# Performance work log

Hardware: AMD Instinct MI355X
Metric: run time of the kernel (lower is better)

## Reference

```python
import jax, jax.numpy as jnp
import numpy as np

B, N, DIM, HEADS, DIM_HEAD = 2, 2048, 1024, 16, 64
INNER = HEADS * DIM_HEAD  # 1024
SCALE = DIM_HEAD ** -0.5
EPS = 1e-5  # fp32 path in the source


def _layernorm_seq(x, g):
    # Faithful to the repo's LayerNorm: statistics over dim=1 (sequence axis),
    # unbiased=False variance, clamp(min=eps).rsqrt(), scale by g over last axis.
    mean = jnp.mean(x, axis=1, keepdims=True)            # [b,1,d]
    var = jnp.mean((x - mean) ** 2, axis=1, keepdims=True)
    return (x - mean) * jax.lax.rsqrt(jnp.maximum(var, EPS)) * g


def setup_inputs() -> dict:
    key = jax.random.key(0)
    ks = jax.random.split(key, 5)
    x = jax.random.normal(ks[0], (B, N, DIM), dtype=jnp.float32)
    rel_pos_bias = jax.random.normal(ks[1], (1, HEADS, N, N), dtype=jnp.float32)
    g = jnp.ones((DIM,), dtype=jnp.float32)
    wq = jax.random.normal(ks[2], (INNER, DIM), dtype=jnp.float32) * (DIM ** -0.5)
    wkv = jax.random.normal(ks[3], (2 * INNER, DIM), dtype=jnp.float32) * (DIM ** -0.5)
    wout = jax.random.normal(ks[4], (DIM, INNER), dtype=jnp.float32) * (INNER ** -0.5)
    return {"x": x, "rel_pos_bias": rel_pos_bias, "g": g, "wq": wq, "wkv": wkv, "wout": wout}


def reference(x, rel_pos_bias, g, wq, wkv, wout):
    # self-attention path: context = x, framerate = None
    xn = _layernorm_seq(x, g)           # [b,n,d]
    cn = xn                              # context is None -> same tensor, same norm
    q = jnp.einsum('bnd,ed->bne', xn, wq)        # [b,n,inner]
    kv = jnp.einsum('bnd,ed->bne', cn, wkv)      # [b,n,2*inner]
    k, v = jnp.split(kv, 2, axis=-1)
    def heads(t):
        return t.reshape(B, N, HEADS, DIM_HEAD).transpose(0, 2, 1, 3)  # b h n d
    q, k, v = heads(q) * SCALE, heads(k), heads(v)
    sim = jnp.einsum('bhid,bhjd->bhij', q, k) + rel_pos_bias
    attn = jax.nn.softmax(sim, axis=-1)
    out = jnp.einsum('bhij,bhjd->bhid', attn, v)
    out = out.transpose(0, 2, 1, 3).reshape(B, N, INNER)  # b n (h d)
    return jnp.einsum('bne,de->bnd', out, wout)
```

## Files before the change

kernel.cpp:

```cpp
#include <hip/hip_runtime.h>
#include <hip/hip_bf16.h>
#include <stdint.h>

#define B_ 2
#define N_ 2048
#define DIM_ 1024
#define HEADS_ 16
#define DH_ 64
#define EPS_ 1e-5f

typedef __attribute__((ext_vector_type(4))) float f32x4;
typedef __attribute__((ext_vector_type(8))) float f32x8;
typedef __attribute__((ext_vector_type(16))) float f32x16;
typedef __attribute__((ext_vector_type(8))) __bf16 bf16x8;
typedef __attribute__((ext_vector_type(4))) unsigned int u32x4;
typedef __attribute__((ext_vector_type(2))) unsigned int u32x2;

__device__ __forceinline__ f32x4 mfma16(bf16x8 a, bf16x8 b, f32x4 c) {
  return __builtin_amdgcn_mfma_f32_16x16x32_bf16(a, b, c, 0, 0, 0);
}

__device__ __forceinline__ f32x16 mfma32(bf16x8 a, bf16x8 b, f32x16 c) {
  return __builtin_amdgcn_mfma_f32_32x32x16_bf16(a, b, c, 0, 0, 0);
}

__device__ __forceinline__ unsigned short f2bf(float x) {
  unsigned int u = __builtin_bit_cast(unsigned int, x);
  u += 0x7fffu + ((u >> 16) & 1u);
  return (unsigned short)(u >> 16);
}

__device__ __forceinline__ unsigned int cvt_pk_bf16(float lo, float hi) {
  unsigned int r;
  asm("v_cvt_pk_bf16_f32 %0, %1, %2" : "=v"(r) : "v"(lo), "v"(hi));
  return r;
}

__device__ __forceinline__ float uasf(unsigned int u) { return __builtin_bit_cast(float, u); }
__device__ __forceinline__ unsigned int fasu(float f) { return __builtin_bit_cast(unsigned int, f); }

__device__ __forceinline__ bf16x8 ld_frag(const unsigned short* p) {
  u32x4 v = *reinterpret_cast<const u32x4*>(p);
  return __builtin_bit_cast(bf16x8, v);
}

__device__ __forceinline__ void gload_lds16(const unsigned short* g, unsigned short* l) {
  __builtin_amdgcn_global_load_lds((const __attribute__((address_space(1))) void*)g,
                                   (__attribute__((address_space(3))) void*)l, 16, 0, 0);
}

__global__ __launch_bounds__(256) void ln_part(const float* __restrict__ x,
                                               float* __restrict__ ps,
                                               float* __restrict__ pss) {
  const int d = blockIdx.x * 256 + threadIdx.x;
  const int b = blockIdx.y >> 4, sp = blockIdx.y & 15;
  const float* xp = x + (size_t)(b * N_ + sp * 128) * DIM_ + d;
  float s = 0.f, ss = 0.f;
  for (int i = 0; i < 128; ++i) {
    float v = xp[(size_t)i * DIM_];
    s += v;
    ss += v * v;
  }
  int c = b * DIM_ + d;
  ps[sp * (B_ * DIM_) + c] = s;
  pss[sp * (B_ * DIM_) + c] = ss;
}

__global__ void ln_fin(const float* __restrict__ ps, const float* __restrict__ pss,
                       const float* __restrict__ g, float* __restrict__ meanA,
                       float* __restrict__ sclA) {
  int c = blockIdx.x * 256 + threadIdx.x;
  float s = 0.f, ss = 0.f;
#pragma unroll
  for (int sp = 0; sp < 16; ++sp) {
    s += ps[sp * (B_ * DIM_) + c];
    ss += pss[sp * (B_ * DIM_) + c];
  }
  float m = s * (1.f / N_);
  float v = ss * (1.f / N_) - m * m;
  meanA[c] = m;
  sclA[c] = rsqrtf(fmaxf(v, EPS_)) * g[c & (DIM_ - 1)];
}

__global__ __launch_bounds__(256) void ln_apply(const float* __restrict__ x,
                                                const float* __restrict__ meanA,
                                                const float* __restrict__ sclA,
                                                unsigned short* __restrict__ xn) {
  size_t t = (size_t)blockIdx.x * 256 + threadIdx.x;
  size_t base = t * 8;
  int d0 = (int)(base & (DIM_ - 1));
  int b = base >= (size_t)N_ * DIM_;
  int c = b * DIM_ + d0;
  const float4* xp = reinterpret_cast<const float4*>(x + base);
  const float4* mp = reinterpret_cast<const float4*>(meanA + c);
  const float4* sp = reinterpret_cast<const float4*>(sclA + c);
  float4 x0 = xp[0], x1 = xp[1];
  float4 m0 = mp[0], m1 = mp[1];
  float4 s0 = sp[0], s1 = sp[1];
  union {
    unsigned short u[8];
    u32x4 v;
  } o;
  o.u[0] = f2bf((x0.x - m0.x) * s0.x);
  o.u[1] = f2bf((x0.y - m0.y) * s0.y);
  o.u[2] = f2bf((x0.z - m0.z) * s0.z);
  o.u[3] = f2bf((x0.w - m0.w) * s0.w);
  o.u[4] = f2bf((x1.x - m1.x) * s1.x);
  o.u[5] = f2bf((x1.y - m1.y) * s1.y);
  o.u[6] = f2bf((x1.z - m1.z) * s1.z);
  o.u[7] = f2bf((x1.w - m1.w) * s1.w);
  *reinterpret_cast<u32x4*>(xn + base) = o.v;
}

__global__ __launch_bounds__(256) void cast_bf16(const float* __restrict__ src,
                                                 unsigned short* __restrict__ dst, float scale) {
  size_t t = (size_t)blockIdx.x * 256 + threadIdx.x;
  size_t base = t * 8;
  const float4* sp = reinterpret_cast<const float4*>(src + base);
  float4 a = sp[0], b4 = sp[1];
  union {
    unsigned short u[8];
    u32x4 v;
  } o;
  o.u[0] = f2bf(a.x * scale);
  o.u[1] = f2bf(a.y * scale);
  o.u[2] = f2bf(a.z * scale);
  o.u[3] = f2bf(a.w * scale);
  o.u[4] = f2bf(b4.x * scale);
  o.u[5] = f2bf(b4.y * scale);
  o.u[6] = f2bf(b4.z * scale);
  o.u[7] = f2bf(b4.w * scale);
  *reinterpret_cast<u32x4*>(dst + base) = o.v;
}

template <bool OUT_F32>
__global__ __launch_bounds__(256) void gemm_bt(const unsigned short* __restrict__ A,
                                               const unsigned short* __restrict__ W,
                                               void* __restrict__ Cout, int K, int ldc) {
  __shared__ unsigned short sA[128 * 64];
  __shared__ unsigned short sB[128 * 64];
  const int tid = threadIdx.x, lane = tid & 63, w = tid >> 6;
  const int wm = w >> 1, wn = w & 1;
  const int l15 = lane & 15, l4 = lane >> 4;
  const int m0 = blockIdx.y * 128, n0 = blockIdx.x * 128;
  f32x4 acc[4][4] = {};
  for (int kt = 0; kt < K; kt += 64) {
    __syncthreads();
#pragma unroll
    for (int p = 0; p < 4; ++p) {
      int flat = p * 256 + tid;
      int row = flat >> 3, c = flat & 7;
      int cs = c ^ (row & 7);
      gload_lds16(A + (size_t)(m0 + row) * K + kt + cs * 8, sA + (size_t)(p * 256 + w * 64) * 8);
      gload_lds16(W + (size_t)(n0 + row) * K + kt + cs * 8, sB + (size_t)(p * 256 + w * 64) * 8);
    }
    __syncthreads();
#pragma unroll
    for (int kk = 0; kk < 2; ++kk) {
      bf16x8 af[4], bfr[4];
#pragma unroll
      for (int i = 0; i < 4; ++i) {
        int rowA = wm * 64 + i * 16 + l15;
        af[i] = ld_frag(sA + rowA * 64 + (((kk * 4 + l4) ^ (rowA & 7)) * 8));
        int rowB = wn * 64 + i * 16 + l15;
        bfr[i] = ld_frag(sB + rowB * 64 + (((kk * 4 + l4) ^ (rowB & 7)) * 8));
      }
#pragma unroll
      for (int i = 0; i < 4; ++i)
#pragma unroll
        for (int j = 0; j < 4; ++j) acc[i][j] = mfma16(af[i], bfr[j], acc[i][j]);
    }
  }
#pragma unroll
  for (int i = 0; i < 4; ++i)
#pragma unroll
    for (int j = 0; j < 4; ++j)
#pragma unroll
      for (int r = 0; r < 4; ++r) {
        size_t off =
            (size_t)(m0 + wm * 64 + i * 16 + l4 * 4 + r) * ldc + (n0 + wn * 64 + j * 16 + l15);
        if (OUT_F32)
          ((float*)Cout)[off] = acc[i][j][r];
        else
          ((unsigned short*)Cout)[off] = f2bf(acc[i][j][r]);
      }
}

__global__ __launch_bounds__(256) void transpose_v(const unsigned short* __restrict__ qkv,
                                                   unsigned short* __restrict__ Vt) {
  __shared__ unsigned short tt[64][65];
  const int tid = threadIdx.x;
  const int h = blockIdx.y >> 1, b = blockIdx.y & 1;
  const int n0 = blockIdx.x * 64;
  const unsigned short* src = qkv + (size_t)(b * N_ + n0) * 3072 + 2048 + h * 64;
#pragma unroll
  for (int i = 0; i < 16; ++i) {
    int idx = i * 256 + tid;
    int r = idx >> 6, c = idx & 63;
    tt[r][c] = src[(size_t)r * 3072 + c];
  }
  __syncthreads();
  unsigned short* dst = Vt + (size_t)(b * HEADS_ + h) * 64 * N_ + n0;
#pragma unroll
  for (int i = 0; i < 16; ++i) {
    int idx = i * 256 + tid;
    int dh = idx >> 6, nn = idx & 63;
    dst[(size_t)dh * N_ + nn] = tt[nn][dh];
  }
}

__global__ __launch_bounds__(512, 2) void flash_attn(const unsigned short* __restrict__ qkv,
                                                     const float* __restrict__ bias,
                                                     const unsigned short* __restrict__ Vt,
                                                     unsigned short* __restrict__ Oatt) {
  __shared__ unsigned short sK[128 * 64];
  __shared__ unsigned short sV[64 * 128];
  __shared__ float sBias[8][32 * 128];

  const int tid = threadIdx.x, lane = tid & 63, w = tid >> 6;
  const int l31 = lane & 31, hi = lane >> 5;
  const int r = blockIdx.x;
  const int bh = r & 31, iblk = r >> 5;
  const int h = bh & 15, b = bh >> 4;
  const int qbase = iblk * 256 + w * 32;

  const unsigned short* Kg = qkv + (size_t)b * N_ * 3072 + 1024 + h * 64;
  const unsigned short* VtB = Vt + (size_t)(b * HEADS_ + h) * 64 * N_;
  const float* bias_h = bias + (size_t)h * N_ * N_;

  const int kflat0 = tid, kflat1 = 512 + tid;
  const int krow0 = kflat0 >> 3, kc0 = (kflat0 & 7) ^ (krow0 & 7);
  const int krow1 = kflat1 >> 3, kc1 = (kflat1 & 7) ^ (krow1 & 7);
  const int vrow0 = kflat0 >> 4, vc0 = (kflat0 & 15) ^ (vrow0 & 15);
  const int vrow1 = kflat1 >> 4, vc1 = (kflat1 & 15) ^ (vrow1 & 15);
  unsigned short* sKb0 = sK + (size_t)(w * 64) * 8;
  unsigned short* sKb1 = sK + (size_t)(512 + w * 64) * 8;
  unsigned short* sVb0 = sV + (size_t)(w * 64) * 8;
  unsigned short* sVb1 = sV + (size_t)(512 + w * 64) * 8;

#define STAGE_KV(JN)                                                       \
  gload_lds16(Kg + (size_t)((JN) + krow0) * 3072 + kc0 * 8, sKb0);         \
  gload_lds16(Kg + (size_t)((JN) + krow1) * 3072 + kc1 * 8, sKb1);         \
  gload_lds16(VtB + (size_t)vrow0 * N_ + (JN) + vc0 * 8, sVb0);            \
  gload_lds16(VtB + (size_t)vrow1 * N_ + (JN) + vc1 * 8, sVb1);

  float* sBw = sBias[w];
  unsigned short* sBw_us = reinterpret_cast<unsigned short*>(sBw);
  const int brr = lane >> 5, bsl = lane & 31;
  const float* bQ = bias_h + (size_t)qbase * N_;
#define SBI(i, JN)                                                            \
  gload_lds16((const unsigned short*)(bQ + (size_t)(2 * (i) + brr) * N_ +     \
                                      (JN) + ((bsl ^ (2 * (i) + brr)) << 2)), \
              sBw_us + (i) * 512);
#define STAGE_BIAS(JN)                                                     \
  SBI(0, JN) SBI(1, JN) SBI(2, JN) SBI(3, JN) SBI(4, JN) SBI(5, JN)        \
  SBI(6, JN) SBI(7, JN) SBI(8, JN) SBI(9, JN) SBI(10, JN) SBI(11, JN)      \
  SBI(12, JN) SBI(13, JN) SBI(14, JN) SBI(15, JN)

#define LDBIAS(DST, CB)                                                        \
  {                                                                            \
    const float* myB_ = sBw + l31 * 128;                                       \
    f32x4 t0 = *reinterpret_cast<const f32x4*>(myB_ + ((((CB) + 0 + hi) ^ l31) << 2)); \
    f32x4 t1 = *reinterpret_cast<const f32x4*>(myB_ + ((((CB) + 2 + hi) ^ l31) << 2)); \
    f32x4 t2 = *reinterpret_cast<const f32x4*>(myB_ + ((((CB) + 4 + hi) ^ l31) << 2)); \
    f32x4 t3 = *reinterpret_cast<const f32x4*>(myB_ + ((((CB) + 6 + hi) ^ l31) << 2)); \
    f32x8 u0_ = __builtin_shufflevector(t0, t1, 0, 1, 2, 3, 4, 5, 6, 7);       \
    f32x8 u1_ = __builtin_shufflevector(t2, t3, 0, 1, 2, 3, 4, 5, 6, 7);       \
    DST = __builtin_shufflevector(u0_, u1_, 0, 1, 2, 3, 4, 5, 6, 7, 8, 9, 10,  \
                                  11, 12, 13, 14, 15);                         \
  }

#define FRAGK(OUT, ROWB, CH)                                              \
  {                                                                       \
    int row_ = (ROWB) + l31;                                              \
    OUT = ld_frag(sK + row_ * 64 + (((CH) ^ (row_ & 7)) * 8));            \
  }
#define FRAGV(OUT, ROWB, CH)                                              \
  {                                                                       \
    int row_ = (ROWB) + l31;                                              \
    OUT = ld_frag(sV + row_ * 128 + (((CH) ^ (row_ & 15)) * 8));          \
  }

#define PACK2(S, PLO, PHI)                                                 \
  {                                                                        \
    unsigned int w0 = cvt_pk_bf16(S[0], S[1]), w1 = cvt_pk_bf16(S[2], S[3]);     \
    unsigned int w2 = cvt_pk_bf16(S[4], S[5]), w3 = cvt_pk_bf16(S[6], S[7]);     \
    unsigned int w4 = cvt_pk_bf16(S[8], S[9]), w5 = cvt_pk_bf16(S[10], S[11]);   \
    unsigned int w6 = cvt_pk_bf16(S[12], S[13]), w7 = cvt_pk_bf16(S[14], S[15]); \
    auto rA = __builtin_amdgcn_permlane32_swap(w0, w2, false, false);      \
    auto rB = __builtin_amdgcn_permlane32_swap(w1, w3, false, false);      \
    auto rC = __builtin_amdgcn_permlane32_swap(w4, w6, false, false);      \
    auto rD = __builtin_amdgcn_permlane32_swap(w5, w7, false, false);      \
    u32x4 pw;                                                              \
    pw[0] = rA[0]; pw[1] = rB[0]; pw[2] = rA[1]; pw[3] = rB[1];            \
    PLO = __builtin_bit_cast(bf16x8, pw);                                  \
    pw[0] = rC[0]; pw[1] = rD[0]; pw[2] = rC[1]; pw[3] = rD[1];            \
    PHI = __builtin_bit_cast(bf16x8, pw);                                  \
  }

  bf16x8 qf0, qf1, qf2, qf3;
  {
    const unsigned short* Qg =
        qkv + (size_t)(b * N_ + qbase + l31) * 3072 + h * 64 + hi * 8;
    qf0 = ld_frag(Qg);
    qf1 = ld_frag(Qg + 16);
    qf2 = ld_frag(Qg + 32);
    qf3 = ld_frag(Qg + 48);
  }

  f32x16 o0 = {}, o1 = {};
  float m_run = -1e30f, l_run = 0.f;

  STAGE_KV(0)
  STAGE_BIAS(0)

  const int NP = N_ / 128;
  for (int p = 0; p < NP; ++p) {
    asm volatile("s_waitcnt vmcnt(0) lgkmcnt(0)" ::: "memory");
    __builtin_amdgcn_s_barrier();

    f32x16 SA0, SA1, SB0, SB1;
    LDBIAS(SA0, 0)
    LDBIAS(SA1, 8)
    LDBIAS(SB0, 16)
    LDBIAS(SB1, 24)
    asm volatile("s_waitcnt lgkmcnt(0)" ::: "memory");
    __builtin_amdgcn_sched_barrier(0);

    if (p + 1 < NP) {
      const size_t jn = (size_t)(p + 1) * 128;
      STAGE_BIAS(jn)
    }

    __builtin_amdgcn_s_setprio(1);
    {
      bf16x8 kf;
      FRAGK(kf, 0, 0 + hi)  SA0 = mfma32(kf, qf0, SA0);
      FRAGK(kf, 0, 2 + hi)  SA0 = mfma32(kf, qf1, SA0);
      FRAGK(kf, 0, 4 + hi)  SA0 = mfma32(kf, qf2, SA0);
      FRAGK(kf, 0, 6 + hi)  SA0 = mfma32(kf, qf3, SA0);
      FRAGK(kf, 32, 0 + hi) SA1 = mfma32(kf, qf0, SA1);
      FRAGK(kf, 32, 2 + hi) SA1 = mfma32(kf, qf1, SA1);
      FRAGK(kf, 32, 4 + hi) SA1 = mfma32(kf, qf2, SA1);
      FRAGK(kf, 32, 6 + hi) SA1 = mfma32(kf, qf3, SA1);
      FRAGK(kf, 64, 0 + hi) SB0 = mfma32(kf, qf0, SB0);
      FRAGK(kf, 64, 2 + hi) SB0 = mfma32(kf, qf1, SB0);
      FRAGK(kf, 64, 4 + hi) SB0 = mfma32(kf, qf2, SB0);
      FRAGK(kf, 64, 6 + hi) SB0 = mfma32(kf, qf3, SB0);
      FRAGK(kf, 96, 0 + hi) SB1 = mfma32(kf, qf0, SB1);
      FRAGK(kf, 96, 2 + hi) SB1 = mfma32(kf, qf1, SB1);
      FRAGK(kf, 96, 4 + hi) SB1 = mfma32(kf, qf2, SB1);
      FRAGK(kf, 96, 6 + hi) SB1 = mfma32(kf, qf3, SB1);
    }
    __builtin_amdgcn_s_setprio(0);

    float c0 = SA0[0], c1 = SA1[0], c2 = SB0[0], c3 = SB1[0];
#pragma unroll
    for (int i = 1; i < 16; ++i) {
      c0 = fmaxf(c0, SA0[i]);
      c1 = fmaxf(c1, SA1[i]);
      c2 = fmaxf(c2, SB0[i]);
      c3 = fmaxf(c3, SB1[i]);
    }
    float mx = fmaxf(fmaxf(c0, c1), fmaxf(c2, c3));
    {
      auto pr_ = __builtin_amdgcn_permlane32_swap(fasu(mx), fasu(mx), false, false);
      mx = fmaxf(uasf(pr_[0]), uasf(pr_[1]));
    }
    float mn = fmaxf(m_run, mx);
    float alpha = __expf(m_run - mn);
#pragma unroll
    for (int i = 0; i < 16; ++i) {
      SA0[i] = __expf(SA0[i] - mn);
      SA1[i] = __expf(SA1[i] - mn);
      SB0[i] = __expf(SB0[i] - mn);
      SB1[i] = __expf(SB1[i] - mn);
    }
    float r0 = 0.f, r1 = 0.f, r2 = 0.f, r3 = 0.f;
#pragma unroll
    for (int i = 0; i < 16; ++i) {
      r0 += SA0[i];
      r1 += SA1[i];
      r2 += SB0[i];
      r3 += SB1[i];
    }
    float rs = (r0 + r1) + (r2 + r3);
    {
      auto pr_ = __builtin_amdgcn_permlane32_swap(fasu(rs), fasu(rs), false, false);
      rs = uasf(pr_[0]) + uasf(pr_[1]);
    }
    l_run = l_run * alpha + rs;
    m_run = mn;
#pragma unroll
    for (int i = 0; i < 16; ++i) {
      o0[i] *= alpha;
      o1[i] *= alpha;
    }

    bf16x8 pA0, pA1, pA2, pA3, pB0, pB1, pB2, pB3;
    PACK2(SA0, pA0, pA1)
    PACK2(SA1, pA2, pA3)
    PACK2(SB0, pB0, pB1)
    PACK2(SB1, pB2, pB3)

    __builtin_amdgcn_s_setprio(1);
    {
      bf16x8 vf;
      FRAGV(vf, 0, 0 + hi)   o0 = mfma32(vf, pA0, o0);
      FRAGV(vf, 0, 2 + hi)   o0 = mfma32(vf, pA1, o0);
      FRAGV(vf, 0, 4 + hi)   o0 = mfma32(vf, pA2, o0);
      FRAGV(vf, 0, 6 + hi)   o0 = mfma32(vf, pA3, o0);
      FRAGV(vf, 0, 8 + hi)   o0 = mfma32(vf, pB0, o0);
      FRAGV(vf, 0, 10 + hi)  o0 = mfma32(vf, pB1, o0);
      FRAGV(vf, 0, 12 + hi)  o0 = mfma32(vf, pB2, o0);
      FRAGV(vf, 0, 14 + hi)  o0 = mfma32(vf, pB3, o0);
      FRAGV(vf, 32, 0 + hi)  o1 = mfma32(vf, pA0, o1);
      FRAGV(vf, 32, 2 + hi)  o1 = mfma32(vf, pA1, o1);
      FRAGV(vf, 32, 4 + hi)  o1 = mfma32(vf, pA2, o1);
      FRAGV(vf, 32, 6 + hi)  o1 = mfma32(vf, pA3, o1);
      FRAGV(vf, 32, 8 + hi)  o1 = mfma32(vf, pB0, o1);
      FRAGV(vf, 32, 10 + hi) o1 = mfma32(vf, pB1, o1);
      FRAGV(vf, 32, 12 + hi) o1 = mfma32(vf, pB2, o1);
      FRAGV(vf, 32, 14 + hi) o1 = mfma32(vf, pB3, o1);
    }
    __builtin_amdgcn_s_setprio(0);

    asm volatile("s_waitcnt lgkmcnt(0)" ::: "memory");
    __builtin_amdgcn_s_barrier();
    if (p + 1 < NP) {
      const size_t jn = (size_t)(p + 1) * 128;
      STAGE_KV(jn)
    }
  }
#undef STAGE_KV
#undef SBI
#undef STAGE_BIAS
#undef LDBIAS
#undef FRAGK
#undef FRAGV
#undef PACK2

  float inv = 1.f / l_run;
  unsigned short* orow =
      Oatt + (size_t)(b * N_ + qbase + l31) * 1024 + h * 64 + hi * 4;
#pragma unroll
  for (int g = 0; g < 4; ++g) {
    u32x2 pk0;
    pk0[0] = cvt_pk_bf16(o0[g * 4 + 0] * inv, o0[g * 4 + 1] * inv);
    pk0[1] = cvt_pk_bf16(o0[g * 4 + 2] * inv, o0[g * 4 + 3] * inv);
    *reinterpret_cast<u32x2*>(orow + g * 8) = pk0;
    u32x2 pk1;
    pk1[0] = cvt_pk_bf16(o1[g * 4 + 0] * inv, o1[g * 4 + 1] * inv);
    pk1[1] = cvt_pk_bf16(o1[g * 4 + 2] * inv, o1[g * 4 + 3] * inv);
    *reinterpret_cast<u32x2*>(orow + 32 + g * 8) = pk1;
  }
}

extern "C" void kernel_launch(void* const* d_in, const int* in_sizes, int n_in, void* d_out,
                              int out_size, void* d_ws, size_t ws_size, hipStream_t stream) {
  const float* x = (const float*)d_in[0];
  const float* bias = (const float*)d_in[1];
  const float* g = (const float*)d_in[2];
  const float* wq = (const float*)d_in[3];
  const float* wkv = (const float*)d_in[4];
  const float* wout = (const float*)d_in[5];
  float* out = (float*)d_out;

  float* ps = (float*)d_ws;
  float* pss = ps + 16 * B_ * DIM_;
  float* meanA = pss + 16 * B_ * DIM_;
  float* sclA = meanA + B_ * DIM_;
  unsigned short* xn = (unsigned short*)(sclA + B_ * DIM_);
  unsigned short* Wqkv = xn + (size_t)4096 * 1024;
  unsigned short* WoutB = Wqkv + (size_t)3072 * 1024;
  unsigned short* qkvb = WoutB + (size_t)1024 * 1024;
  unsigned short* Vt = qkvb + (size_t)4096 * 3072;
  unsigned short* Oatt = xn;

  ln_part<<<dim3(DIM_ / 256, B_ * 16), 256, 0, stream>>>(x, ps, pss);
  ln_fin<<<dim3((B_ * DIM_) / 256), 256, 0, stream>>>(ps, pss, g, meanA, sclA);
  ln_apply<<<dim3((B_ * N_ * DIM_) / 2048), 256, 0, stream>>>(x, meanA, sclA, xn);
  cast_bf16<<<dim3((DIM_ * DIM_) / 2048), 256, 0, stream>>>(wq, Wqkv, 0.125f);
  cast_bf16<<<dim3((2 * DIM_ * DIM_) / 2048), 256, 0, stream>>>(wkv, Wqkv + (size_t)DIM_ * DIM_,
                                                                1.0f);
  cast_bf16<<<dim3((DIM_ * DIM_) / 2048), 256, 0, stream>>>(wout, WoutB, 1.0f);
  gemm_bt<false><<<dim3(3072 / 128, 4096 / 128), 256, 0, stream>>>(xn, Wqkv, qkvb, DIM_, 3072);
  transpose_v<<<dim3(N_ / 64, B_ * HEADS_), 256, 0, stream>>>(qkvb, Vt);
  flash_attn<<<dim3(256), 512, 0, stream>>>(qkvb, bias, Vt, Oatt);
  gemm_bt<true><<<dim3(1024 / 128, 4096 / 128), 256, 0, stream>>>(Oatt, WoutB, out, DIM_, 1024);
}
```

Measured before the change: 173.8 us.

## Double-buffer LDS tiles in gemm_bt to overlap global loads with MFMA

Changes the GEMM main loop to keep two LDS stages. The next K-tile is prefetched with direct-to-LDS loads while MFMAs consume the current one, and each iteration ends with a single waitcnt plus barrier. This targets the exposed global-load latency in the projection GEMMs. LDS use per block doubles to 64KB, which may cut occupancy. The raw s_barrier relies on the vmcnt wait to order the LDS writes.

```diff
diff --git a/kernel.cpp b/kernel.cpp
--- a/kernel.cpp
+++ b/kernel.cpp
@@ -137,40 +137,57 @@
 __global__ __launch_bounds__(256) void gemm_bt(const unsigned short* __restrict__ A,
                                                const unsigned short* __restrict__ W,
                                                void* __restrict__ Cout, int K, int ldc) {
-  __shared__ unsigned short sA[128 * 64];
-  __shared__ unsigned short sB[128 * 64];
+  __shared__ unsigned short sA[2][128 * 64];
+  __shared__ unsigned short sB[2][128 * 64];
   const int tid = threadIdx.x, lane = tid & 63, w = tid >> 6;
   const int wm = w >> 1, wn = w & 1;
   const int l15 = lane & 15, l4 = lane >> 4;
   const int m0 = blockIdx.y * 128, n0 = blockIdx.x * 128;
   f32x4 acc[4][4] = {};
-  for (int kt = 0; kt < K; kt += 64) {
-    __syncthreads();
-#pragma unroll
-    for (int p = 0; p < 4; ++p) {
-      int flat = p * 256 + tid;
-      int row = flat >> 3, c = flat & 7;
-      int cs = c ^ (row & 7);
-      gload_lds16(A + (size_t)(m0 + row) * K + kt + cs * 8, sA + (size_t)(p * 256 + w * 64) * 8);
-      gload_lds16(W + (size_t)(n0 + row) * K + kt + cs * 8, sB + (size_t)(p * 256 + w * 64) * 8);
-    }
-    __syncthreads();
+
+#define GSTAGE(S, KT)                                                          \
+  {                                                                            \
+    _Pragma("unroll") for (int p = 0; p < 4; ++p) {                            \
+      int flat = p * 256 + tid;                                                \
+      int row = flat >> 3, c = flat & 7;                                       \
+      int cs = c ^ (row & 7);                                                  \
+      gload_lds16(A + (size_t)(m0 + row) * K + (KT) + cs * 8,                  \
+                  sA[S] + (size_t)(p * 256 + w * 64) * 8);                     \
+      gload_lds16(W + (size_t)(n0 + row) * K + (KT) + cs * 8,                  \
+                  sB[S] + (size_t)(p * 256 + w * 64) * 8);                     \
+    }                                                                          \
+  }
+
+  GSTAGE(0, 0)
+  asm volatile("s_waitcnt vmcnt(0)" ::: "memory");
+  __builtin_amdgcn_s_barrier();
+
+  const int NKT = K / 64;
+  for (int ki = 0; ki < NKT; ++ki) {
+    const int cur = ki & 1;
+    if (ki + 1 < NKT) GSTAGE(cur ^ 1, (ki + 1) * 64)
+    const unsigned short* cA = sA[cur];
+    const unsigned short* cB = sB[cur];
 #pragma unroll
     for (int kk = 0; kk < 2; ++kk) {
       bf16x8 af[4], bfr[4];
 #pragma unroll
       for (int i = 0; i < 4; ++i) {
         int rowA = wm * 64 + i * 16 + l15;
-        af[i] = ld_frag(sA + rowA * 64 + (((kk * 4 + l4) ^ (rowA & 7)) * 8));
+        af[i] = ld_frag(cA + rowA * 64 + (((kk * 4 + l4) ^ (rowA & 7)) * 8));
         int rowB = wn * 64 + i * 16 + l15;
-        bfr[i] = ld_frag(sB + rowB * 64 + (((kk * 4 + l4) ^ (rowB & 7)) * 8));
+        bfr[i] = ld_frag(cB + rowB * 64 + (((kk * 4 + l4) ^ (rowB & 7)) * 8));
       }
 #pragma unroll
       for (int i = 0; i < 4; ++i)
 #pragma unroll
         for (int j = 0; j < 4; ++j) acc[i][j] = mfma16(af[i], bfr[j], acc[i][j]);
     }
-  }
+    asm volatile("s_waitcnt vmcnt(0)" ::: "memory");
+    __builtin_amdgcn_s_barrier();
+  }
+#undef GSTAGE
+
 #pragma unroll
   for (int i = 0; i < 4; ++i)
 #pragma unroll
```

New measurement: 176.8 us. About the same (+1.7%).
